# Performance work log

Measured on AMD Instinct MI355X. Metric: run time of the kernel, lower is better.

## Reference

```python
import jax, jax.numpy as jnp
import numpy as np

N = 100000   # nodes
E = 800000   # edges
D = 64       # hidden_channels
H = 4        # heads
C = D        # out_channels per head (PyG: out_channels=hidden)


def setup_inputs() -> dict:
    key = jax.random.key(0)
    ks = jax.random.split(key, 20)
    inp = {}
    inp['x'] = jax.random.normal(ks[0], (N, D), dtype=jnp.float32)
    inp['edge_index'] = jax.random.randint(ks[1], (2, E), 0, N, dtype=jnp.int32)
    i = 2
    for layer in (1, 2):
        for nm in ('Wq', 'Wk', 'Wv'):
            inp[f'{nm}{layer}'] = jax.random.normal(ks[i], (D, H * C), dtype=jnp.float32) * 0.05; i += 1
            inp[f'b{nm[1]}{layer}'] = jnp.zeros((H * C,), dtype=jnp.float32)
        inp[f'Ws{layer}'] = jax.random.normal(ks[i], (D, D), dtype=jnp.float32) * 0.05; i += 1
        inp[f'bs{layer}'] = jnp.zeros((D,), dtype=jnp.float32)
    return inp


def _transformer_conv(x, src, dst, Wq, bq, Wk, bk, Wv, bv, Ws, bs):
    n = x.shape[0]
    q = (x @ Wq + bq).reshape(n, H, C)
    k = (x @ Wk + bk).reshape(n, H, C)
    v = (x @ Wv + bv).reshape(n, H, C)
    # per-edge attention logits: [E, H]
    alpha = jnp.einsum('ehc,ehc->eh', q[dst], k[src]) / np.sqrt(C).astype(np.float32)
    # segment softmax over incoming edges of each destination node
    amax = jax.ops.segment_max(alpha, dst, num_segments=n)          # [N, H]
    ex = jnp.exp(alpha - amax[dst])                                 # [E, H]
    denom = jax.ops.segment_sum(ex, dst, num_segments=n)           # [N, H]
    attn = ex / (denom[dst] + 1e-16)                                # [E, H]
    msg = v[src] * attn[:, :, None]                                 # [E, H, C]
    agg = jax.ops.segment_sum(msg, dst, num_segments=n)            # [N, H, C]
    # concat=False -> mean over heads; root_weight skip connection
    return agg.mean(axis=1) + x @ Ws + bs


def reference(x, edge_index, Wq1, bq1, Wk1, bk1, Wv1, bv1, Ws1, bs1,
              Wq2, bq2, Wk2, bk2, Wv2, bv2, Ws2, bs2):
    src, dst = edge_index[0], edge_index[1]
    h = _transformer_conv(x, src, dst, Wq1, bq1, Wk1, bk1, Wv1, bv1, Ws1, bs1)
    h = jax.nn.relu(h)
    out = _transformer_conv(h, src, dst, Wq2, bq2, Wk2, bk2, Wv2, bv2, Ws2, bs2)
    return out
```

## Files before the change

### kernel.cpp

```cpp
#include <hip/hip_runtime.h>
#include <hip/hip_fp16.h>
#include <math.h>


typedef __attribute__((ext_vector_type(8))) short bf16x8;
typedef __attribute__((ext_vector_type(4))) float f32x4;
typedef __attribute__((ext_vector_type(2))) float f32x2;

#define QKSCALE 32.0f
#define C_EXP2 1.760325e-4f

__device__ inline unsigned short f2bf(float f) {
    unsigned int u = __float_as_uint(f);
    u = (u + 0x7fffu + ((u >> 16) & 1u)) >> 16;
    return (unsigned short)u;
}

#if __has_builtin(__builtin_amdgcn_cvt_pk_fp8_f32) && __has_builtin(__builtin_amdgcn_cvt_pk_f32_fp8)
#define HW_FP8 1
#endif

#ifndef HW_FP8
__device__ inline unsigned int fp8_enc1(float f) {
    unsigned int u = __float_as_uint(f);
    unsigned int s = (u >> 24) & 0x80u;
    float a = fabsf(f);
    if (a >= 448.f) return s | 0x7Eu;
    if (a < 0.015625f) return s;
    unsigned int ua = __float_as_uint(a);
    unsigned int r = ua + 0x7FFFFu + ((ua >> 20) & 1u);
    int e = (int)((r >> 23) & 255u) - 120;
    unsigned int m = (r >> 20) & 7u;
    if (e < 1) return s;
    if (e > 15) return s | 0x7Eu;
    return s | (unsigned int)((e << 3) | m);
}
__device__ inline float fp8_dec1(unsigned int b) {
    unsigned int e = (b >> 3) & 15u, m = b & 7u;
    float v;
    if (e) v = __uint_as_float(((e + 120u) << 23) | (m << 20));
    else   v = (float)m * 0.001953125f;
    return (b & 0x80u) ? -v : v;
}
#endif

__device__ inline unsigned int fp8x4_pack(float f0, float f1, float f2, float f3) {
#ifdef HW_FP8
    int pk = __builtin_amdgcn_cvt_pk_fp8_f32(f0, f1, 0, false);
    pk = __builtin_amdgcn_cvt_pk_fp8_f32(f2, f3, pk, true);
    return (unsigned int)pk;
#else
    return fp8_enc1(f0) | (fp8_enc1(f1) << 8) | (fp8_enc1(f2) << 16) | (fp8_enc1(f3) << 24);
#endif
}

__device__ inline unsigned int i8x4_pack(float f0, float f1, float f2, float f3) {
    int a = (int)rintf(f0 * QKSCALE); a = a < -127 ? -127 : (a > 127 ? 127 : a);
    int b = (int)rintf(f1 * QKSCALE); b = b < -127 ? -127 : (b > 127 ? 127 : b);
    int c = (int)rintf(f2 * QKSCALE); c = c < -127 ? -127 : (c > 127 ? 127 : c);
    int d = (int)rintf(f3 * QKSCALE); d = d < -127 ? -127 : (d > 127 ? 127 : d);
    return (unsigned int)((a & 255) | ((b & 255) << 8) | ((c & 255) << 16) | ((d & 255) << 24));
}

__device__ inline int sdot4(unsigned int a, unsigned int b, int c) {
#if __has_builtin(__builtin_amdgcn_sdot4)
    return __builtin_amdgcn_sdot4((int)a, (int)b, c, false);
#else
    int r = c;
#pragma unroll
    for (int i = 0; i < 4; ++i) {
        int ai = (int)(a << (24 - 8 * i)) >> 24;
        int bi = (int)(b << (24 - 8 * i)) >> 24;
        r += ai * bi;
    }
    return r;
#endif
}

__global__ void k_setup(
    const float* __restrict__ x, unsigned short* __restrict__ Xb, int ncast4,
    const float* __restrict__ Wq1, const float* __restrict__ Wk1,
    const float* __restrict__ Wv1, const float* __restrict__ Ws1,
    const float* __restrict__ Wq2, const float* __restrict__ Wk2,
    const float* __restrict__ Wv2, const float* __restrict__ Ws2,
    unsigned short* __restrict__ Wt,
    int* __restrict__ counts, int N, int castBl)
{
    int b = blockIdx.x, tid = threadIdx.x;
    if (b < castBl) {
        int i = b * 256 + tid;
        if (i < ncast4) {
            float4 v = ((const float4*)x)[i];
            ushort4 o;
            o.x = f2bf(v.x); o.y = f2bf(v.y); o.z = f2bf(v.z); o.w = f2bf(v.w);
            ((ushort4*)Xb)[i] = o;
        }
    } else if (b < castBl + 416) {
        int j = (b - castBl) * 256 + tid;
        int layer = j / 53248;
        int r = j % 53248;
        if (r < 49152) {
            int m = r / 16384, w = r % 16384;
            int n = w / 64, k = w % 64;
            const float* W = (layer == 0)
                ? ((m == 0) ? Wq1 : (m == 1) ? Wk1 : Wv1)
                : ((m == 0) ? Wq2 : (m == 1) ? Wk2 : Wv2);
            Wt[layer * 53248 + m * 16384 + n * 64 + k] = f2bf(W[k * 256 + n]);
        } else {
            int w = r - 49152;
            int n = w / 64, k = w % 64;
            const float* W = (layer == 0) ? Ws1 : Ws2;
            Wt[layer * 53248 + 49152 + n * 64 + k] = f2bf(W[k * 64 + n]);
        }
    } else {
        int i = (b - castBl - 416) * 256 + tid;
        if (i < N) counts[i] = 0;
    }
}

#define SCAN_B 256
#define SCAN_CHUNK 2048
__global__ void k_scan1(const int* __restrict__ counts, int n,
                        int* __restrict__ offs, int* __restrict__ bsums) {
    __shared__ int lds[SCAN_B];
    int b = blockIdx.x, tid = threadIdx.x;
    int base = b * SCAN_CHUNK + tid * 8;
    int v[8]; int s = 0;
#pragma unroll
    for (int i = 0; i < 8; ++i) { int idx = base + i; int c = (idx < n) ? counts[idx] : 0; v[i] = s; s += c; }
    lds[tid] = s;
    for (int off = 1; off < SCAN_B; off <<= 1) {
        __syncthreads();
        int x = (tid >= off) ? lds[tid - off] : 0;
        __syncthreads();
        lds[tid] += x;
    }
    __syncthreads();
    int texcl = lds[tid] - s;
#pragma unroll
    for (int i = 0; i < 8; ++i) { int idx = base + i; if (idx < n) offs[idx] = texcl + v[i]; }
    if (tid == SCAN_B - 1) bsums[b] = lds[tid];
}

__global__ void k_scan2(int* bsums, int nb) {
    __shared__ int lds[256];
    int t = threadIdx.x;
    if (nb > 256) {
        if (t == 0) { int s = 0; for (int i = 0; i < nb; ++i) { int c = bsums[i]; bsums[i] = s; s += c; } }
        return;
    }
    int v = (t < nb) ? bsums[t] : 0;
    lds[t] = v;
    for (int off = 1; off < 256; off <<= 1) {
        __syncthreads();
        int x = (t >= off) ? lds[t - off] : 0;
        __syncthreads();
        lds[t] += x;
    }
    __syncthreads();
    if (t < nb) bsums[t] = lds[t] - v;
}

__global__ void k_scatter(const int* __restrict__ src, const int* __restrict__ dst, int E,
                          const int* __restrict__ offs, const int* __restrict__ bsums,
                          const int* __restrict__ rank, int* __restrict__ csr_src) {
    int e = blockIdx.x * 256 + threadIdx.x;
    if (e < E) {
        int d = dst[e];
        csr_src[offs[d] + bsums[d >> 11] + rank[e]] = src[e];
    }
}

#define GST 68
__global__ __launch_bounds__(256, 2) void k_gemm(
    const unsigned short* __restrict__ Xb, int nrows,
    const unsigned short* __restrict__ WtL,
    const float* __restrict__ bqp, const float* __restrict__ bkp,
    const float* __restrict__ bvp, const float* __restrict__ bsp,
    unsigned char* __restrict__ Qp, unsigned char* __restrict__ Kp,
    unsigned char* __restrict__ Vp, unsigned char* __restrict__ Sp,
    const int* __restrict__ dstp, int histE,
    int* __restrict__ counts, int* __restrict__ rank, int gemmBl, int ntiles)
{
    __shared__ unsigned char st[4][64 * GST];
    __shared__ float bias[832];
    int tid = threadIdx.x;
    if (blockIdx.x >= gemmBl) {
        int e = (blockIdx.x - gemmBl) * 256 + tid;
        if (e < histE) rank[e] = atomicAdd(&counts[dstp[e]], 1);
        return;
    }
    int qtr = tid >> 6, lane = tid & 63;
    int quad = lane >> 4, n16 = lane & 15;
    unsigned char* wst = st[qtr];

    if (tid < 208) {
        float4 b4;
        if (tid < 64)       b4 = ((const float4*)bqp)[tid];
        else if (tid < 128) b4 = ((const float4*)bkp)[tid - 64];
        else if (tid < 192) b4 = ((const float4*)bvp)[tid - 128];
        else                b4 = ((const float4*)bsp)[tid - 192];
        ((float4*)bias)[tid] = b4;
    }

    const unsigned short* Wq = WtL;
    const unsigned short* Wk = WtL + 16384;
    const unsigned short* Wv = WtL + 32768;
    const unsigned short* Ws = WtL + 49152;
    bf16x8 fQ[8], fK[8], fV[8], fS[2];
#pragma unroll
    for (int c = 0; c < 4; ++c) {
        int roff = ((qtr * 4 + c) * 16 + n16) * 64 + quad * 8;
        fQ[2 * c]     = *(const bf16x8*)(Wq + roff);
        fQ[2 * c + 1] = *(const bf16x8*)(Wq + roff + 32);
        fK[2 * c]     = *(const bf16x8*)(Wk + roff);
        fK[2 * c + 1] = *(const bf16x8*)(Wk + roff + 32);
        fV[2 * c]     = *(const bf16x8*)(Wv + roff);
        fV[2 * c + 1] = *(const bf16x8*)(Wv + roff + 32);
    }
    {
        int roff = (qtr * 16 + n16) * 64 + quad * 8;
        fS[0] = *(const bf16x8*)(Ws + roff);
        fS[1] = *(const bf16x8*)(Ws + roff + 32);
    }
    __syncthreads();

    auto loadA = [&](int t, bf16x8 (&x0)[4], bf16x8 (&x1)[4]) {
        int r0 = t * 64;
#pragma unroll
        for (int g = 0; g < 4; ++g) {
            int node = r0 + g * 16 + n16;
            int nodec = (node < nrows) ? node : (nrows - 1);
            x0[g] = *(const bf16x8*)(Xb + (size_t)nodec * 64 + quad * 8);
            x1[g] = *(const bf16x8*)(Xb + (size_t)nodec * 64 + 32 + quad * 8);
        }
    };

    auto do_mat = [&](const bf16x8 (&fm)[8], int boff, unsigned char* plane,
                      bool isInt8, int r0,
                      const bf16x8 (&x0)[4], const bf16x8 (&x1)[4]) {
#pragma unroll
        for (int c = 0; c < 4; ++c) {
            float4 cb = *(const float4*)(bias + boff + qtr * 64 + c * 16 + quad * 4);
#pragma unroll
            for (int g = 0; g < 4; ++g) {
                f32x4 acc = {cb.x, cb.y, cb.z, cb.w};
                acc = __builtin_amdgcn_mfma_f32_16x16x32_bf16(fm[2 * c],     x0[g], acc, 0, 0, 0);
                acc = __builtin_amdgcn_mfma_f32_16x16x32_bf16(fm[2 * c + 1], x1[g], acc, 0, 0, 0);
                unsigned int pk = isInt8 ? i8x4_pack(acc[0], acc[1], acc[2], acc[3])
                                         : fp8x4_pack(acc[0], acc[1], acc[2], acc[3]);
                *(unsigned int*)(wst + (g * 16 + n16) * GST + c * 16 + quad * 4) = pk;
            }
        }
#pragma unroll
        for (int it = 0; it < 4; ++it) {
            int row = it * 16 + (lane >> 2);
            uint4 v = *(const uint4*)(wst + row * GST + (lane & 3) * 16);
            int nd = r0 + row;
            if (nd < nrows)
                *(uint4*)(plane + (size_t)nd * 256 + qtr * 64 + (lane & 3) * 16) = v;
        }
    };

    bf16x8 a0[4], a1[4], b0[4], b1[4];
    int t = blockIdx.x;
    if (t < ntiles) loadA(t, a0, a1);
    for (; t < ntiles; t += gemmBl) {
        int tn = t + gemmBl;
        if (tn < ntiles) loadA(tn, b0, b1);
        int r0 = t * 64;
        do_mat(fQ, 0,   Qp, true,  r0, a0, a1);
        do_mat(fK, 256, Kp, true,  r0, a0, a1);
        do_mat(fV, 512, Vp, false, r0, a0, a1);
        {
            float4 cs = *(const float4*)(bias + 768 + qtr * 16 + quad * 4);
#pragma unroll
            for (int g = 0; g < 4; ++g) {
                f32x4 acc = {cs.x, cs.y, cs.z, cs.w};
                acc = __builtin_amdgcn_mfma_f32_16x16x32_bf16(fS[0], a0[g], acc, 0, 0, 0);
                acc = __builtin_amdgcn_mfma_f32_16x16x32_bf16(fS[1], a1[g], acc, 0, 0, 0);
                *(float4*)(wst + (g * 16 + n16) * GST + quad * 16) =
                    make_float4(acc[0], acc[1], acc[2], acc[3]);
            }
#pragma unroll
            for (int it = 0; it < 4; ++it) {
                int row = it * 16 + (lane >> 2);
                uint4 v = *(const uint4*)(wst + row * GST + (lane & 3) * 16);
                int nd = r0 + row;
                if (nd < nrows)
                    *(uint4*)(Sp + (size_t)nd * 256 + qtr * 64 + (lane & 3) * 16) = v;
            }
        }
#pragma unroll
        for (int g = 0; g < 4; ++g) { a0[g] = b0[g]; a1[g] = b1[g]; }
    }
}

__global__ __launch_bounds__(256) void k_attn(
    const unsigned char* __restrict__ Qp, const unsigned char* __restrict__ Kp,
    const unsigned char* __restrict__ Vp, const float* __restrict__ Sp,
    const int* __restrict__ offs, const int* __restrict__ bsums,
    const int* __restrict__ csr_src,
    float* __restrict__ out, unsigned short* __restrict__ Xb,
    int n, int Etot, int mode)
{
    int node = blockIdx.x * 4 + (threadIdx.x >> 6);
    if (node >= n) return;
    int lane = threadIdx.x & 63;
    int sl = lane & 31;
    int half = lane >> 5;
    unsigned slb = (unsigned)sl * 8u;
    uint2 q8 = *(const uint2*)(Qp + ((unsigned)node << 8) + slb);
    int beg = offs[node] + bsums[node >> 11];
    int end = (node + 1 < n) ? (offs[node + 1] + bsums[(node + 1) >> 11]) : Etot;
    float l = 0.f;
    f32x2 acc2[4];
#pragma unroll
    for (int i = 0; i < 4; ++i) acc2[i] = (f32x2){0.f, 0.f};
    int my = (beg + lane < end) ? csr_src[beg + lane] : 0;
    for (int base = beg; base < end; base += 8) {
        int myn = (base + 8 + lane < end) ? csr_src[base + 8 + lane] : 0;
        int cnt = end - base; if (cnt > 8) cnt = 8;
        uint2 kk[4], vv[4];
#pragma unroll
        for (int p = 0; p < 4; ++p) {
            int idx = __shfl(my, 2 * p + half);
            unsigned off = ((unsigned)idx << 8) + slb;
            kk[p] = *(const uint2*)(Kp + off);
            vv[p] = *(const uint2*)(Vp + off);
        }
#pragma unroll
        for (int p = 0; p < 4; ++p) {
            int d = sdot4(kk[p].x, q8.x, 0);
            d = sdot4(kk[p].y, q8.y, d);
            d += __shfl_xor(d, 1); d += __shfl_xor(d, 2); d += __shfl_xor(d, 4);
            float w = __builtin_exp2f((float)d * C_EXP2);
            w = (2 * p + half < cnt) ? w : 0.f;
            l += w;
            f32x2 w2 = {w, w};
#ifdef HW_FP8
            f32x2 va = __builtin_amdgcn_cvt_pk_f32_fp8((int)vv[p].x, false);
            f32x2 vb = __builtin_amdgcn_cvt_pk_f32_fp8((int)vv[p].x, true);
            f32x2 vc = __builtin_amdgcn_cvt_pk_f32_fp8((int)vv[p].y, false);
            f32x2 vd = __builtin_amdgcn_cvt_pk_f32_fp8((int)vv[p].y, true);
#else
            f32x2 va = {fp8_dec1(vv[p].x & 255u), fp8_dec1((vv[p].x >> 8) & 255u)};
            f32x2 vb = {fp8_dec1((vv[p].x >> 16) & 255u), fp8_dec1(vv[p].x >> 24)};
            f32x2 vc = {fp8_dec1(vv[p].y & 255u), fp8_dec1((vv[p].y >> 8) & 255u)};
            f32x2 vd = {fp8_dec1((vv[p].y >> 16) & 255u), fp8_dec1(vv[p].y >> 24)};
#endif
            acc2[0] = __builtin_elementwise_fma(va, w2, acc2[0]);
            acc2[1] = __builtin_elementwise_fma(vb, w2, acc2[1]);
            acc2[2] = __builtin_elementwise_fma(vc, w2, acc2[2]);
            acc2[3] = __builtin_elementwise_fma(vd, w2, acc2[3]);
        }
        my = myn;
    }
    float acc[8] = {acc2[0][0], acc2[0][1], acc2[1][0], acc2[1][1],
                    acc2[2][0], acc2[2][1], acc2[3][0], acc2[3][1]};
    l += __shfl_xor(l, 32);
#pragma unroll
    for (int i = 0; i < 8; ++i) acc[i] += __shfl_xor(acc[i], 32);
    float inv = 1.f / (l + 1e-16f);
#pragma unroll
    for (int i = 0; i < 8; ++i) acc[i] *= inv;
#pragma unroll
    for (int i = 0; i < 8; ++i) {
        acc[i] += __shfl_xor(acc[i], 8);
        acc[i] += __shfl_xor(acc[i], 16);
        acc[i] *= 0.25f;
    }
    if (lane < 8) {
        const float* Srow = Sp + ((size_t)node << 6);
        float4 s0 = *(const float4*)(Srow + lane * 8);
        float4 s1 = *(const float4*)(Srow + lane * 8 + 4);
        float r0 = acc[0] + s0.x, r1 = acc[1] + s0.y;
        float r2 = acc[2] + s0.z, r3 = acc[3] + s0.w;
        float r4 = acc[4] + s1.x, r5 = acc[5] + s1.y;
        float r6 = acc[6] + s1.z, r7 = acc[7] + s1.w;
        if (mode == 1) {
            r0 = fmaxf(r0, 0.f); r1 = fmaxf(r1, 0.f);
            r2 = fmaxf(r2, 0.f); r3 = fmaxf(r3, 0.f);
            r4 = fmaxf(r4, 0.f); r5 = fmaxf(r5, 0.f);
            r6 = fmaxf(r6, 0.f); r7 = fmaxf(r7, 0.f);
            uint4 o;
            o.x = (unsigned int)f2bf(r0) | ((unsigned int)f2bf(r1) << 16);
            o.y = (unsigned int)f2bf(r2) | ((unsigned int)f2bf(r3) << 16);
            o.z = (unsigned int)f2bf(r4) | ((unsigned int)f2bf(r5) << 16);
            o.w = (unsigned int)f2bf(r6) | ((unsigned int)f2bf(r7) << 16);
            *(uint4*)(Xb + (size_t)node * 64 + lane * 8) = o;
        } else {
            *(float4*)(out + (size_t)node * 64 + lane * 8) = make_float4(r0, r1, r2, r3);
            *(float4*)(out + (size_t)node * 64 + lane * 8 + 4) = make_float4(r4, r5, r6, r7);
        }
    }
}

extern "C" void kernel_launch(void* const* d_in, const int* in_sizes, int n_in,
                              void* d_out, int out_size, void* d_ws, size_t ws_size,
                              hipStream_t stream)
{
    const float* x  = (const float*)d_in[0];
    const int*   ei = (const int*)d_in[1];
    int N = in_sizes[0] / 64;
    int E = in_sizes[1] / 2;
    const int* srcp = ei;
    const int* dstp = ei + E;
    const float* Wq1 = (const float*)d_in[2],  *bq1 = (const float*)d_in[3];
    const float* Wk1 = (const float*)d_in[4],  *bk1 = (const float*)d_in[5];
    const float* Wv1 = (const float*)d_in[6],  *bv1 = (const float*)d_in[7];
    const float* Ws1 = (const float*)d_in[8],  *bs1 = (const float*)d_in[9];
    const float* Wq2 = (const float*)d_in[10], *bq2 = (const float*)d_in[11];
    const float* Wk2 = (const float*)d_in[12], *bk2 = (const float*)d_in[13];
    const float* Wv2 = (const float*)d_in[14], *bv2 = (const float*)d_in[15];
    const float* Ws2 = (const float*)d_in[16], *bs2 = (const float*)d_in[17];
    float* out = (float*)d_out;

    char* ws = (char*)d_ws;
    size_t off = 0;
    auto alloc = [&](size_t bytes) -> void* {
        void* p = ws + off;
        off = (off + bytes + 255) & ~(size_t)255;
        return p;
    };
    unsigned short* Xb = (unsigned short*)alloc((size_t)N * 64 * 2);
    unsigned char* Qp  = (unsigned char*)alloc(((size_t)N + 64) * 256);
    unsigned char* Kp  = (unsigned char*)alloc(((size_t)N + 64) * 256);
    unsigned char* Vp  = (unsigned char*)alloc(((size_t)N + 64) * 256);
    unsigned char* Sp  = (unsigned char*)alloc(((size_t)N + 64) * 256);
    unsigned short* Wt = (unsigned short*)alloc(2 * 53248 * 2);
    int* counts = (int*)alloc((size_t)N * 4);
    int* rank   = (int*)alloc((size_t)E * 4);
    int* offs   = (int*)alloc((size_t)N * 4);
    int* bsums  = (int*)alloc(1024 * 4);
    int* csr    = (int*)alloc((size_t)E * 4);
    (void)n_in; (void)out_size;
    if (off > ws_size) return;

    int ebl = (E + 255) / 256;
    int nb_scan = (N + SCAN_CHUNK - 1) / SCAN_CHUNK;
    int ntiles = (N + 63) / 64;
    int gemm_bl = ntiles < 512 ? ntiles : 512;
    int hist_bl = (E + 255) / 256;
    int attn_bl = (N + 3) / 4;
    int ncast4 = N * 16;
    int castBl = (ncast4 + 255) / 256;
    int zeroBl = (N + 255) / 256;

    k_setup<<<castBl + 416 + zeroBl, 256, 0, stream>>>(
        x, Xb, ncast4, Wq1, Wk1, Wv1, Ws1, Wq2, Wk2, Wv2, Ws2, Wt, counts, N, castBl);

    k_gemm<<<gemm_bl + hist_bl, 256, 0, stream>>>(
        Xb, N, Wt, bq1, bk1, bv1, bs1, Qp, Kp, Vp, Sp,
        dstp, E, counts, rank, gemm_bl, ntiles);

    k_scan1<<<nb_scan, SCAN_B, 0, stream>>>(counts, N, offs, bsums);
    k_scan2<<<1, 256, 0, stream>>>(bsums, nb_scan);
    k_scatter<<<ebl, 256, 0, stream>>>(srcp, dstp, E, offs, bsums, rank, csr);

    k_attn<<<attn_bl, 256, 0, stream>>>(Qp, Kp, Vp, (const float*)Sp,
                                        offs, bsums, csr, out, Xb, N, E, 1);

    k_gemm<<<gemm_bl, 256, 0, stream>>>(
        Xb, N, Wt + 53248, bq2, bk2, bv2, bs2, Qp, Kp, Vp, Sp,
        dstp, 0, counts, rank, gemm_bl, ntiles);

    k_attn<<<attn_bl, 256, 0, stream>>>(Qp, Kp, Vp, (const float*)Sp,
                                        offs, bsums, csr, out, Xb, N, E, 0);
}
```

Before: 362.3 us.

## Split Q/K/V/S planes into per-head sub-planes and raise GEMM grid cap

Stores each head's 64-byte slice of Q, K, V and the skip output in its own contiguous sub-plane (head-major) instead of interleaving 256-byte rows per node. The aim is a smaller memory footprint per gather: each edge's K/V fetch for a given head now touches compact 64-byte rows, which should improve cache and TLB locality across the gather-heavy attention kernel. It also doubles the GEMM persistent-block cap from 512 to 1024. In exchange, each node's four head slices are now spread across four distant regions, so one node's data no longer sits in a single cache line.

```diff
diff --git a/kernel.cpp b/kernel.cpp
--- a/kernel.cpp
+++ b/kernel.cpp
@@ -173,7 +173,7 @@
 
 #define GST 68
 __global__ __launch_bounds__(256, 2) void k_gemm(
-    const unsigned short* __restrict__ Xb, int nrows,
+    const unsigned short* __restrict__ Xb, int nrows, int npad,
     const unsigned short* __restrict__ WtL,
     const float* __restrict__ bqp, const float* __restrict__ bkp,
     const float* __restrict__ bvp, const float* __restrict__ bsp,
@@ -192,6 +192,8 @@
     }
     int qtr = tid >> 6, lane = tid & 63;
     int quad = lane >> 4, n16 = lane & 15;
+    unsigned subpl = (unsigned)npad * 64u;
+    unsigned qbase = (unsigned)qtr * subpl;
     unsigned char* wst = st[qtr];
 
     if (tid < 208) {
@@ -258,7 +260,7 @@
             uint4 v = *(const uint4*)(wst + row * GST + (lane & 3) * 16);
             int nd = r0 + row;
             if (nd < nrows)
-                *(uint4*)(plane + (size_t)nd * 256 + qtr * 64 + (lane & 3) * 16) = v;
+                *(uint4*)(plane + qbase + (unsigned)nd * 64u + (lane & 3) * 16) = v;
         }
     };
 
@@ -288,7 +290,7 @@
                 uint4 v = *(const uint4*)(wst + row * GST + (lane & 3) * 16);
                 int nd = r0 + row;
                 if (nd < nrows)
-                    *(uint4*)(Sp + (size_t)nd * 256 + qtr * 64 + (lane & 3) * 16) = v;
+                    *(uint4*)(Sp + qbase + (unsigned)nd * 64u + (lane & 3) * 16) = v;
             }
         }
 #pragma unroll
@@ -298,19 +300,20 @@
 
 __global__ __launch_bounds__(256) void k_attn(
     const unsigned char* __restrict__ Qp, const unsigned char* __restrict__ Kp,
-    const unsigned char* __restrict__ Vp, const float* __restrict__ Sp,
+    const unsigned char* __restrict__ Vp, const unsigned char* __restrict__ Sp,
     const int* __restrict__ offs, const int* __restrict__ bsums,
     const int* __restrict__ csr_src,
     float* __restrict__ out, unsigned short* __restrict__ Xb,
-    int n, int Etot, int mode)
+    int n, int npad, int Etot, int mode)
 {
     int node = blockIdx.x * 4 + (threadIdx.x >> 6);
     if (node >= n) return;
     int lane = threadIdx.x & 63;
     int sl = lane & 31;
     int half = lane >> 5;
-    unsigned slb = (unsigned)sl * 8u;
-    uint2 q8 = *(const uint2*)(Qp + ((unsigned)node << 8) + slb);
+    unsigned subpl = (unsigned)npad * 64u;
+    unsigned gb = (unsigned)(sl >> 3) * subpl + (unsigned)(sl & 7) * 8u;
+    uint2 q8 = *(const uint2*)(Qp + gb + ((unsigned)node << 6));
     int beg = offs[node] + bsums[node >> 11];
     int end = (node + 1 < n) ? (offs[node + 1] + bsums[(node + 1) >> 11]) : Etot;
     float l = 0.f;
@@ -325,7 +328,7 @@
 #pragma unroll
         for (int p = 0; p < 4; ++p) {
             int idx = __shfl(my, 2 * p + half);
-            unsigned off = ((unsigned)idx << 8) + slb;
+            unsigned off = gb + ((unsigned)idx << 6);
             kk[p] = *(const uint2*)(Kp + off);
             vv[p] = *(const uint2*)(Vp + off);
         }
@@ -371,9 +374,10 @@
         acc[i] *= 0.25f;
     }
     if (lane < 8) {
-        const float* Srow = Sp + ((size_t)node << 6);
-        float4 s0 = *(const float4*)(Srow + lane * 8);
-        float4 s1 = *(const float4*)(Srow + lane * 8 + 4);
+        unsigned soff = (unsigned)(lane >> 1) * subpl + (unsigned)(lane & 1) * 32u
+                      + ((unsigned)node << 6);
+        float4 s0 = *(const float4*)(Sp + soff);
+        float4 s1 = *(const float4*)(Sp + soff + 16);
         float r0 = acc[0] + s0.x, r1 = acc[1] + s0.y;
         float r2 = acc[2] + s0.z, r3 = acc[3] + s0.w;
         float r4 = acc[4] + s1.x, r5 = acc[5] + s1.y;
@@ -416,6 +420,8 @@
     const float* Ws2 = (const float*)d_in[16], *bs2 = (const float*)d_in[17];
     float* out = (float*)d_out;
 
+    int npad = N + 64;
+
     char* ws = (char*)d_ws;
     size_t off = 0;
     auto alloc = [&](size_t bytes) -> void* {
@@ -424,10 +430,10 @@
         return p;
     };
     unsigned short* Xb = (unsigned short*)alloc((size_t)N * 64 * 2);
-    unsigned char* Qp  = (unsigned char*)alloc(((size_t)N + 64) * 256);
-    unsigned char* Kp  = (unsigned char*)alloc(((size_t)N + 64) * 256);
-    unsigned char* Vp  = (unsigned char*)alloc(((size_t)N + 64) * 256);
-    unsigned char* Sp  = (unsigned char*)alloc(((size_t)N + 64) * 256);
+    unsigned char* Qp  = (unsigned char*)alloc((size_t)npad * 256);
+    unsigned char* Kp  = (unsigned char*)alloc((size_t)npad * 256);
+    unsigned char* Vp  = (unsigned char*)alloc((size_t)npad * 256);
+    unsigned char* Sp  = (unsigned char*)alloc((size_t)npad * 256);
     unsigned short* Wt = (unsigned short*)alloc(2 * 53248 * 2);
     int* counts = (int*)alloc((size_t)N * 4);
     int* rank   = (int*)alloc((size_t)E * 4);
@@ -440,7 +446,7 @@
     int ebl = (E + 255) / 256;
     int nb_scan = (N + SCAN_CHUNK - 1) / SCAN_CHUNK;
     int ntiles = (N + 63) / 64;
-    int gemm_bl = ntiles < 512 ? ntiles : 512;
+    int gemm_bl = ntiles < 1024 ? ntiles : 1024;
     int hist_bl = (E + 255) / 256;
     int attn_bl = (N + 3) / 4;
     int ncast4 = N * 16;
@@ -451,20 +457,20 @@
         x, Xb, ncast4, Wq1, Wk1, Wv1, Ws1, Wq2, Wk2, Wv2, Ws2, Wt, counts, N, castBl);
 
     k_gemm<<<gemm_bl + hist_bl, 256, 0, stream>>>(
-        Xb, N, Wt, bq1, bk1, bv1, bs1, Qp, Kp, Vp, Sp,
+        Xb, N, npad, Wt, bq1, bk1, bv1, bs1, Qp, Kp, Vp, Sp,
         dstp, E, counts, rank, gemm_bl, ntiles);
 
     k_scan1<<<nb_scan, SCAN_B, 0, stream>>>(counts, N, offs, bsums);
     k_scan2<<<1, 256, 0, stream>>>(bsums, nb_scan);
     k_scatter<<<ebl, 256, 0, stream>>>(srcp, dstp, E, offs, bsums, rank, csr);
 
-    k_attn<<<attn_bl, 256, 0, stream>>>(Qp, Kp, Vp, (const float*)Sp,
-                                        offs, bsums, csr, out, Xb, N, E, 1);
+    k_attn<<<attn_bl, 256, 0, stream>>>(Qp, Kp, Vp, Sp,
+                                        offs, bsums, csr, out, Xb, N, npad, E, 1);
 
     k_gemm<<<gemm_bl, 256, 0, stream>>>(
-        Xb, N, Wt + 53248, bq2, bk2, bv2, bs2, Qp, Kp, Vp, Sp,
+        Xb, N, npad, Wt + 53248, bq2, bk2, bv2, bs2, Qp, Kp, Vp, Sp,
         dstp, 0, counts, rank, gemm_bl, ntiles);
 
-    k_attn<<<attn_bl, 256, 0, stream>>>(Qp, Kp, Vp, (const float*)Sp,
-                                        offs, bsums, csr, out, Xb, N, E, 0);
-}
+    k_attn<<<attn_bl, 256, 0, stream>>>(Qp, Kp, Vp, Sp,
+                                        offs, bsums, csr, out, Xb, N, npad, E, 0);
+}
```

Result: slower. 475.1 us (+31.1%).
